# Optimization experiments

Hardware: AMD Instinct MI355X
Metric: run time of the kernel (lower is better)

Reference implementation:

```python
import jax, jax.numpy as jnp
import numpy as np

B = 128        # graphs per batch
N = 512        # nodes per graph (equal-size graphs -> dense mask all True)
F_IN = 128     # dataset.num_features
HID = 128      # hidden
C3 = 3 * HID   # num_layers * hidden (pool in_channels)
HEADS = 5
NC = 2         # num_classes
KC = NC + 1    # num_clusters2 = num_clusters_per_class*(num_classes+1) = 3
NC1 = NC       # num_clusters1 = num_clusters_per_class*num_classes = 2
OUT = 16       # pool out_channels
EPER = 8192    # edges per graph
TAU = 1.0
L1, L2 = 10.0, 0.01
BN_EPS = 1e-5


def setup_inputs() -> dict:
    key = jax.random.key(0)
    ks = jax.random.split(key, 12)
    Nn = B * N
    E = B * EPER
    x = jax.random.normal(ks[0], (Nn, F_IN), jnp.float32)
    local = jax.random.randint(ks[1], (2, E), 0, N)
    off = (jnp.repeat(jnp.arange(B), EPER) * N)[None, :]
    edge_index = (local + off).astype(jnp.int64)  # global node ids, per-graph blocks
    y = jax.random.randint(ks[2], (B,), 0, NC).astype(jnp.int64)

    def w(k_, shp, fan):
        return (jax.random.normal(k_, shp, jnp.float32) / np.sqrt(fan)).astype(jnp.float32)

    params = dict(
        W1=w(ks[3], (F_IN, HID), F_IN), b1=jnp.zeros((HID,), jnp.float32),
        W2=w(ks[4], (HID, HID), HID), b2=jnp.zeros((HID,), jnp.float32),
        W3=w(ks[5], (HID, HID), HID), b3=jnp.zeros((HID,), jnp.float32),
        bn_gamma=jnp.ones((C3,), jnp.float32), bn_beta=jnp.zeros((C3,), jnp.float32),
        k=w(ks[6], (HEADS, KC, C3), C3),
        lin_pool_W=w(ks[7], (C3, OUT), C3),
        lin1_W=w(ks[8], (NC1 * OUT, HID), NC1 * OUT), lin1_b=jnp.zeros((HID,), jnp.float32),
        lin2_W=w(ks[9], (HID, NC), HID), lin2_b=jnp.zeros((NC,), jnp.float32),
    )
    return dict(x=x, edge_index=edge_index, y=y, **params)


def reference(x, edge_index, y, W1, b1, W2, b2, W3, b3, bn_gamma, bn_beta, k,
              lin_pool_W, lin1_W, lin1_b, lin2_W, lin2_b):
    src, dst = edge_index[0], edge_index[1]
    Nn = x.shape[0]

    # GCNConv (normalize=False): out[dst] += (h @ W)[src] ; + bias
    def gcn(h, W, b):
        m = h @ W
        return jnp.zeros_like(m).at[dst].add(m[src]) + b

    h1 = jax.nn.relu(gcn(x, W1, b1))
    h2 = jax.nn.relu(gcn(h1, W2, b2))
    h3 = jax.nn.relu(gcn(h2, W3, b3))
    X = jnp.concatenate([h1, h2, h3], axis=1)  # [Nn, C3]

    # BatchNorm1d (training-mode batch stats, biased var)
    mu = X.mean(0)
    var = X.var(0)
    Xn = (X - mu) / jnp.sqrt(var + BN_EPS) * bn_gamma + bn_beta

    # --- IMPO pool ---
    H, K, C = k.shape
    k2 = k.reshape(H * K, C)
    # squared euclidean cdist: [H*K, Nn]
    d2 = jnp.maximum((k2 ** 2).sum(-1)[:, None] + (Xn ** 2).sum(-1)[None, :]
                     - 2.0 * (k2 @ Xn.T), 0.0)
    dist = (1.0 + d2 / TAU) ** (-(TAU + 1.0) / 2.0)
    dist = dist.reshape(H, K, B, N).transpose(2, 0, 3, 1)  # [B,H,N,K]
    Sh = dist / dist.sum(-1, keepdims=True)
    S = Sh.sum(1)  # sum over heads -> [B,N,K]; mask is all-True

    # per-graph adjacency aggregation: out[row] += S[col], then degree norm
    Sf = S.reshape(Nn, K)
    Sagg = jnp.zeros_like(Sf).at[src].add(Sf[dst])
    deg = (jnp.zeros((Nn,), Sf.dtype).at[src].add(1.0).at[dst].add(1.0)) / 2.0
    deg = jnp.where(deg == 0, 1.0, deg)
    S_raw = (Sagg / deg[:, None]).reshape(B, N, K)

    # use_gumbel=False path: softmax + hard argmax mask
    g = jax.nn.softmax(S_raw, axis=-1)
    onehot = jax.nn.one_hot(jnp.argmax(g, -1), K, dtype=g.dtype)
    Sfin = g * onehot

    xd = Xn.reshape(B, N, C)
    xp = jnp.einsum('bnk,bnc->bkc', Sfin, xd) @ lin_pool_W  # [B,K,OUT]
    out_x = xp[:, :NC1, :]

    # --- impo_loss ---
    yb = jnp.broadcast_to(y[:, None], (B, N))
    assigned = jnp.argmax(Sfin, -1)
    ac = assigned  # cluster_map is identity for num_clusters_per_class=1
    mr = (ac < NC) & (ac == yb)
    mw = (ac < NC) & (ac != yb)
    sum_loss = Sfin.sum(1)[:, :NC1].sum(1).mean()
    mf = (mr | mw).astype(Sfin.dtype)
    counts = jnp.zeros((NC,), Sfin.dtype).at[yb.reshape(-1)].add(mf.reshape(-1))
    bc = jnp.ones((NC,), Sfin.dtype) + counts
    weight = bc.max() / (bc + 0.001)
    logits = Sfin[..., :KC - 1]  # drop last cluster column
    logp = jax.nn.log_softmax(logits, axis=-1)
    ce = -jnp.take_along_axis(logp, yb[..., None], axis=-1)[..., 0]
    wsamp = weight[yb] * mf
    cel = (wsamp * ce).sum() / jnp.maximum(wsamp.sum(), 1e-12)
    total_loss = L1 * cel + L2 * sum_loss

    # head
    xf = out_x.reshape(B, -1)
    xf = jax.nn.relu(xf @ lin1_W + lin1_b)
    out = jax.nn.log_softmax(xf @ lin2_W + lin2_b, axis=-1)
    return (out, total_loss)
```

## Files before the change

### kernel.cpp

```cpp
#include <hip/hip_runtime.h>
#include <hip/hip_bf16.h>

#define BB 128
#define NV 512
#define NN (BB*NV)
#define EPER_C 8192
#define E_TOT (BB*EPER_C)
#define BN_EPS_F 1e-5f

typedef unsigned int u32;
typedef unsigned short u16;

__device__ __forceinline__ float bfu2f_lo(u32 w) { return __uint_as_float(w << 16); }
__device__ __forceinline__ float bfu2f_hi(u32 w) { return __uint_as_float(w & 0xFFFF0000u); }
__device__ __forceinline__ u16 f2bf(float f) {
    u32 u = __float_as_uint(f);
    u32 r = (u + 0x7FFFu + ((u >> 16) & 1u)) >> 16;
    return (u16)r;
}
__device__ __forceinline__ u32 pack2(float a, float b) {
    return (u32)f2bf(a) | ((u32)f2bf(b) << 16);
}
__device__ __forceinline__ float f16u2f(u16 h) {
    const u32 s = ((u32)h & 0x8000u) << 16;
    const u32 e = (h >> 10) & 0x1Fu;
    const u32 m = h & 0x3FFu;
    if (e == 0u) {
        float v = (float)m * 5.9604644775390625e-8f;
        return s ? -v : v;
    }
    if (e == 31u) return __uint_as_float(s | 0x7F800000u | (m << 13));
    return __uint_as_float(s | ((e + 112u) << 23) | (m << 13));
}
__device__ __forceinline__ void u32tof2(u32 w, u32 cls, float& f0, float& f1) {
    if (cls == 2u) { f0 = f16u2f((u16)(w & 0xFFFFu)); f1 = f16u2f((u16)(w >> 16)); }
    else { f0 = bfu2f_lo(w); f1 = bfu2f_hi(w); }
}
__device__ __forceinline__ float san(float v) {
    if (!(v == v)) return 0.f;
    return fminf(fmaxf(v, -1e30f), 1e30f);
}

__device__ __forceinline__ float2 h_ld2(const u32* H, size_t i2, int hf32) {
    float2 v;
    if (hf32) {
        v = ((const float2*)H)[i2];
    } else {
        const u32 w = H[i2];
        v.x = bfu2f_lo(w);
        v.y = bfu2f_hi(w);
    }
    return v;
}
__device__ __forceinline__ void h_st2(u32* H, size_t i2, float a, float b, int hf32) {
    if (hf32) {
        float2 v;
        v.x = a;
        v.y = b;
        ((float2*)H)[i2] = v;
    } else {
        H[i2] = pack2(a, b);
    }
}
__device__ __forceinline__ float h_ld1(const u32* H, size_t i, int hf32) {
    if (hf32) return ((const float*)H)[i];
    return __uint_as_float(((u32)((const u16*)H)[i]) << 16);
}

__global__ void fill_out_kernel(float* o, float v) {
    int i = blockIdx.x * 256 + threadIdx.x;
    if (i < 257) o[i] = v;
}

__global__ void init_kernel(u32* p, int n) {
    int i = blockIdx.x * 256 + threadIdx.x;
    if (i < n) p[i] = 0u;
}

__global__ void probe_kernel(const u32* g, const u32* e, u32* flags) {
    const int t = threadIdx.x;
    u32 acc = 0u;
    for (int i = t; i < 2048; i += 64) acc |= e[2 * i + 1];
#pragma unroll
    for (int s = 32; s > 0; s >>= 1) acc |= (u32)__shfl_xor((int)acc, s);
    if (t == 0) {
        const u32 w = g[0];
        u32 cls = 0u;
        if (w == 0x3F800000u) cls = 1u;
        else if (w == 0x3C003C00u) cls = 2u;
        flags[9] = cls;
        flags[8] = (acc != 0u) ? 1u : 0u;
    }
}

__device__ __forceinline__ int ld_src(const int* e, int is64, size_t i) {
    return (is64 ? e[2 * i] : e[i]) & (NN - 1);
}
__device__ __forceinline__ int ld_dst(const int* e, int is64, size_t i) {
    return (is64 ? e[2 * ((size_t)E_TOT + i)] : e[(size_t)E_TOT + i]) & (NN - 1);
}
__device__ __forceinline__ int ld_y(const int* y, int is64, int bi) {
    return (is64 ? y[2 * bi] : y[bi]) & 1;
}

#define CVT_TOT 66690
struct CvtPtrs { const void* p[14]; };
__global__ __launch_bounds__(256) void cvt_all_kernel(CvtPtrs ptrs, float* __restrict__ dst,
                                                      const u32* __restrict__ flags) {
    const int i = blockIdx.x * 256 + threadIdx.x;
    if (i >= CVT_TOT) return;
    const int kPof[14] = {0, 16384, 16512, 32896, 33024, 49408, 49536, 49920,
                          50304, 56064, 62208, 66304, 66432, 66688};
    const void* pp = ptrs.p[0];
    int base = 0;
#pragma unroll
    for (int s2 = 1; s2 < 14; ++s2) {
        if (i >= kPof[s2]) { pp = ptrs.p[s2]; base = kPof[s2]; }
    }
    const int off = i - base;
    const u32 cls = flags[9];
    float v;
    if (cls == 1u) v = ((const float*)pp)[off];
    else if (cls == 2u) v = f16u2f(((const u16*)pp)[off]);
    else v = __uint_as_float(((u32)((const u16*)pp)[off]) << 16);
    dst[i] = v;
}

__global__ __launch_bounds__(512) void csr_kernel(const int* __restrict__ eidx,
                                                  const u32* __restrict__ flags,
                                                  u16* __restrict__ sortedD,
                                                  u32* __restrict__ rpD) {
    __shared__ u32 cntD[512];
    __shared__ u32 offD[512];
    __shared__ u32 p[512];
    const int bi = blockIdx.x;
    const int t = threadIdx.x;
    const int is64 = (flags[8] == 0u);
    cntD[t] = 0u;
    __syncthreads();
    const size_t eb = (size_t)bi * EPER_C;
    for (int e = t; e < EPER_C; e += 512) {
        const int dl = ld_dst(eidx, is64, eb + e) & 511;
        atomicAdd(&cntD[dl], 1u);
    }
    __syncthreads();
    p[t] = cntD[t];
    __syncthreads();
    for (int d = 1; d < 512; d <<= 1) {
        u32 va = p[t];
        if (t >= d) va += p[t - d];
        __syncthreads();
        p[t] = va;
        __syncthreads();
    }
    offD[t] = p[t] - cntD[t];
    __syncthreads();
    rpD[bi * 513 + t] = offD[t];
    if (t == 0) rpD[bi * 513 + 512] = EPER_C;
    cntD[t] = 0u;
    __syncthreads();
    for (int e = t; e < EPER_C; e += 512) {
        const int sl = ld_src(eidx, is64, eb + e) & 511;
        const int dl = ld_dst(eidx, is64, eb + e) & 511;
        const u32 pos = offD[dl] + atomicAdd(&cntD[dl], 1u);
        sortedD[eb + pos] = (u16)sl;
    }
}

__global__ __launch_bounds__(512, 4) void gemm_k(const u32* __restrict__ X2,
                                                 const float* __restrict__ Wc,
                                                 u32* __restrict__ Y2,
                                                 const u32* __restrict__ flags,
                                                 int xmode, int hf32) {
    __shared__ float xsT[2][32][132];
    __shared__ float ws[2][32][128];
    const int n0 = blockIdx.x * 128;
    const int t = threadIdx.x;
    const int tx = t & 31, ty = t >> 5;
    u32 cls;
    if (xmode) cls = flags[9];
    else cls = hf32 ? 1u : 0u;

    float4 px[2];
    uint4 pxu;
    float4 pw[2];

#define GLOADX(kc) do { \
    if (cls == 1u) { \
        const float4* Xf4 = (const float4*)X2; \
_Pragma("unroll") \
        for (int i_ = 0; i_ < 2; ++i_) { \
            const int task = t + i_ * 512; \
            const int r_ = task >> 3, q_ = task & 7; \
            px[i_] = Xf4[(size_t)(n0 + r_) * 32 + (kc) * 8 + q_]; \
        } \
    } else { \
        const uint4* Xu4 = (const uint4*)X2; \
        const int r_ = t >> 2, uq_ = t & 3; \
        pxu = Xu4[(size_t)(n0 + r_) * 16 + (kc) * 4 + uq_]; \
    } \
} while (0)

#define GLOADW(kc) do { \
    const float4* Wf4 = (const float4*)Wc; \
_Pragma("unroll") \
    for (int i_ = 0; i_ < 2; ++i_) { \
        const int task = t + i_ * 512; \
        const int kr_ = task >> 5, cq_ = task & 31; \
        pw[i_] = Wf4[(size_t)((kc) * 32 + kr_) * 32 + cq_]; \
    } \
} while (0)

#define SWRITE(bi) do { \
    if (cls == 1u) { \
_Pragma("unroll") \
        for (int i_ = 0; i_ < 2; ++i_) { \
            const int task = t + i_ * 512; \
            const int r_ = task >> 3, q_ = task & 7; \
            xsT[bi][4 * q_ + 0][r_] = px[i_].x; \
            xsT[bi][4 * q_ + 1][r_] = px[i_].y; \
            xsT[bi][4 * q_ + 2][r_] = px[i_].z; \
            xsT[bi][4 * q_ + 3][r_] = px[i_].w; \
        } \
    } else { \
        const int r_ = t >> 2, uq_ = t & 3; \
        const u32* wp_ = (const u32*)&pxu; \
_Pragma("unroll") \
        for (int m_ = 0; m_ < 4; ++m_) { \
            float f0_, f1_; \
            u32tof2(wp_[m_], cls, f0_, f1_); \
            xsT[bi][uq_ * 8 + 2 * m_ + 0][r_] = f0_; \
            xsT[bi][uq_ * 8 + 2 * m_ + 1][r_] = f1_; \
        } \
    } \
_Pragma("unroll") \
    for (int i_ = 0; i_ < 2; ++i_) { \
        const int task = t + i_ * 512; \
        const int kr_ = task >> 5, cq_ = task & 31; \
        *(float4*)&ws[bi][kr_][4 * cq_] = pw[i_]; \
    } \
} while (0)

    GLOADX(0);
    GLOADW(0);
    SWRITE(0);
    __syncthreads();

    float a[2][4][4];
#pragma unroll
    for (int rh = 0; rh < 2; ++rh)
#pragma unroll
        for (int j = 0; j < 4; ++j)
#pragma unroll
            for (int i = 0; i < 4; ++i) a[rh][j][i] = 0.f;

    for (int c = 0; c < 4; ++c) {
        if (c < 3) {
            GLOADX(c + 1);
            GLOADW(c + 1);
        }
        const float (*xb)[132] = xsT[c & 1];
        const float (*wb)[128] = ws[c & 1];
#pragma unroll 8
        for (int k = 0; k < 32; ++k) {
            const float4 xa = *(const float4*)&xb[k][8 * ty];
            const float4 xc = *(const float4*)&xb[k][8 * ty + 4];
            const float4 wv = *(const float4*)&wb[k][4 * tx];
            const float xr0[4] = {xa.x, xa.y, xa.z, xa.w};
            const float xr1[4] = {xc.x, xc.y, xc.z, xc.w};
#pragma unroll
            for (int j = 0; j < 4; ++j) {
                a[0][j][0] += xr0[j] * wv.x;
                a[0][j][1] += xr0[j] * wv.y;
                a[0][j][2] += xr0[j] * wv.z;
                a[0][j][3] += xr0[j] * wv.w;
                a[1][j][0] += xr1[j] * wv.x;
                a[1][j][1] += xr1[j] * wv.y;
                a[1][j][2] += xr1[j] * wv.z;
                a[1][j][3] += xr1[j] * wv.w;
            }
        }
        if (c < 3) {
            SWRITE((c + 1) & 1);
            __syncthreads();
        }
    }
#undef GLOADX
#undef GLOADW
#undef SWRITE

#pragma unroll
    for (int rh = 0; rh < 2; ++rh) {
#pragma unroll
        for (int j = 0; j < 4; ++j) {
            const size_t n = (size_t)n0 + 8 * ty + 4 * rh + j;
            if (hf32) {
                float4 o;
                o.x = a[rh][j][0]; o.y = a[rh][j][1];
                o.z = a[rh][j][2]; o.w = a[rh][j][3];
                ((float4*)Y2)[n * 32 + tx] = o;
            } else {
                Y2[n * 64 + 2 * tx + 0] = pack2(a[rh][j][0], a[rh][j][1]);
                Y2[n * 64 + 2 * tx + 1] = pack2(a[rh][j][2], a[rh][j][3]);
            }
        }
    }
}

__global__ __launch_bounds__(1024) void gcn_lds_k(const u16* __restrict__ sortedD,
                                                  const u32* __restrict__ rpD,
                                                  const float* __restrict__ bias,
                                                  u32* __restrict__ M2,
                                                  float* __restrict__ bnacc,
                                                  int col_base, int hf32) {
    __shared__ float Ms[512 * 64];
    __shared__ u32 srt32[EPER_C / 2];
    __shared__ u32 rp[513];
    const int t = threadIdx.x;
    const int bi = blockIdx.x >> 1;
    const int hf = blockIdx.x & 1;
    const size_t rowbase = (size_t)bi * 512;
    const u16* srt = (const u16*)srt32;

    const u32* srcw = (const u32*)(sortedD + (size_t)bi * EPER_C);
    for (int i = t; i < EPER_C / 2; i += 1024) srt32[i] = srcw[i];
    for (int i = t; i < 513; i += 1024) rp[i] = rpD[bi * 513 + i];

    if (hf32) {
        const float4* src4 = (const float4*)M2;
        float4* dst4 = (float4*)Ms;
        for (int idx = t; idx < 512 * 16; idx += 1024) {
            const int r = idx >> 4, q = idx & 15;
            dst4[r * 16 + q] = src4[(rowbase + r) * 32 + hf * 16 + q];
        }
    } else {
        for (int idx = t; idx < 512 * 32; idx += 1024) {
            const int r = idx >> 5, q = idx & 31;
            const u32 w = M2[(rowbase + r) * 64 + hf * 32 + q];
            Ms[r * 64 + 2 * q] = bfu2f_lo(w);
            Ms[r * 64 + 2 * q + 1] = bfu2f_hi(w);
        }
    }
    __syncthreads();

    const int j = t & 15;
    const int g = t >> 4;
    const float4* M4 = (const float4*)Ms;
    const float bx = bias[hf * 64 + j * 4 + 0];
    const float by = bias[hf * 64 + j * 4 + 1];
    const float bz = bias[hf * 64 + j * 4 + 2];
    const float bw = bias[hf * 64 + j * 4 + 3];
    float S0 = 0.f, S1 = 0.f, S2 = 0.f, S3 = 0.f;
    float Q0 = 0.f, Q1 = 0.f, Q2 = 0.f, Q3 = 0.f;

#pragma unroll
    for (int gi = 0; gi < 8; ++gi) {
        const int l = g + gi * 64;
        u32 r1 = rp[l + 1];
        if (r1 > EPER_C) r1 = EPER_C;
        u32 r0 = rp[l];
        if (r0 > r1) r0 = r1;
        float ax = 0.f, ay = 0.f, az = 0.f, aw = 0.f;
        u32 idx = r0;
        for (; idx + 8 <= r1; idx += 8) {
            const int s0 = srt[idx];
            const int s1 = srt[idx + 1];
            const int s2 = srt[idx + 2];
            const int s3 = srt[idx + 3];
            const int s4 = srt[idx + 4];
            const int s5 = srt[idx + 5];
            const int s6 = srt[idx + 6];
            const int s7 = srt[idx + 7];
            const float4 v0 = M4[s0 * 16 + j];
            const float4 v1 = M4[s1 * 16 + j];
            const float4 v2 = M4[s2 * 16 + j];
            const float4 v3 = M4[s3 * 16 + j];
            const float4 v4 = M4[s4 * 16 + j];
            const float4 v5 = M4[s5 * 16 + j];
            const float4 v6 = M4[s6 * 16 + j];
            const float4 v7 = M4[s7 * 16 + j];
            ax += (v0.x + v1.x) + (v2.x + v3.x) + (v4.x + v5.x) + (v6.x + v7.x);
            ay += (v0.y + v1.y) + (v2.y + v3.y) + (v4.y + v5.y) + (v6.y + v7.y);
            az += (v0.z + v1.z) + (v2.z + v3.z) + (v4.z + v5.z) + (v6.z + v7.z);
            aw += (v0.w + v1.w) + (v2.w + v3.w) + (v4.w + v5.w) + (v6.w + v7.w);
        }
        for (; idx + 4 <= r1; idx += 4) {
            const int sa = srt[idx];
            const int sb = srt[idx + 1];
            const int sc = srt[idx + 2];
            const int sd = srt[idx + 3];
            const float4 va = M4[sa * 16 + j];
            const float4 vb = M4[sb * 16 + j];
            const float4 vc = M4[sc * 16 + j];
            const float4 vd = M4[sd * 16 + j];
            ax += va.x + vb.x; ay += va.y + vb.y; az += va.z + vb.z; aw += va.w + vb.w;
            ax += vc.x + vd.x; ay += vc.y + vd.y; az += vc.z + vd.z; aw += vc.w + vd.w;
        }
        for (; idx < r1; ++idx) {
            const int sa = srt[idx];
            const float4 va = M4[sa * 16 + j];
            ax += va.x; ay += va.y; az += va.z; aw += va.w;
        }
        float vx = san(ax + bx); vx = vx > 0.f ? vx : 0.f;
        float vy = san(ay + by); vy = vy > 0.f ? vy : 0.f;
        float vz = san(az + bz); vz = vz > 0.f ? vz : 0.f;
        float vw = san(aw + bw); vw = vw > 0.f ? vw : 0.f;
        if (hf32) {
            float4 o; o.x = vx; o.y = vy; o.z = vz; o.w = vw;
            ((float4*)M2)[(rowbase + l) * 32 + hf * 16 + j] = o;
        } else {
            const size_t pr = (rowbase + l) * 64 + hf * 32 + 2 * j;
            M2[pr] = pack2(vx, vy);
            M2[pr + 1] = pack2(vz, vw);
        }
        S0 += vx; S1 += vy; S2 += vz; S3 += vw;
        Q0 += vx * vx; Q1 += vy * vy; Q2 += vz * vz; Q3 += vw * vw;
    }

    S0 += __shfl_xor(S0, 16); Q0 += __shfl_xor(Q0, 16);
    S1 += __shfl_xor(S1, 16); Q1 += __shfl_xor(Q1, 16);
    S2 += __shfl_xor(S2, 16); Q2 += __shfl_xor(Q2, 16);
    S3 += __shfl_xor(S3, 16); Q3 += __shfl_xor(Q3, 16);
    S0 += __shfl_xor(S0, 32); Q0 += __shfl_xor(Q0, 32);
    S1 += __shfl_xor(S1, 32); Q1 += __shfl_xor(Q1, 32);
    S2 += __shfl_xor(S2, 32); Q2 += __shfl_xor(Q2, 32);
    S3 += __shfl_xor(S3, 32); Q3 += __shfl_xor(Q3, 32);

    __syncthreads();
    float* red = (float*)srt32;
    const int lane = t & 63;
    const int wid = t >> 6;
    if (lane < 16) {
        float* rw = &red[(wid * 16 + j) * 8];
        rw[0] = S0; rw[1] = Q0; rw[2] = S1; rw[3] = Q1;
        rw[4] = S2; rw[5] = Q2; rw[6] = S3; rw[7] = Q3;
    }
    __syncthreads();
    if (t < 128) {
        float s = 0.f;
        for (int w = 0; w < 16; ++w) s += red[w * 128 + t];
        const int jj = t >> 3;
        const int cc = (t >> 1) & 3;
        const int st = t & 1;
        atomicAdd(&bnacc[(size_t)(col_base + hf * 64 + jj * 4 + cc) * 2 + st], s);
    }
}

__global__ __launch_bounds__(384) void bn2_kernel(const float* __restrict__ bnacc,
                                                  const float* __restrict__ gamma,
                                                  const float* __restrict__ beta,
                                                  float* __restrict__ scaleA,
                                                  float* __restrict__ shiftA) {
    const int c = threadIdx.x;
    const float s = bnacc[c * 2 + 0];
    const float s2 = bnacc[c * 2 + 1];
    const float inv_n = 1.f / (float)NN;
    const float mu = san(s * inv_n);
    float var = san(s2 * inv_n - mu * mu);
    var = var > 0.f ? var : 0.f;
    const float sc = san(gamma[c] / sqrtf(var + BN_EPS_F));
    scaleA[c] = sc;
    shiftA[c] = san(beta[c] - mu * sc);
}

__global__ __launch_bounds__(256) void dist_kernel(const u32* __restrict__ h1,
                                                   const u32* __restrict__ h2,
                                                   const u32* __restrict__ h3,
                                                   const float* __restrict__ kc,
                                                   const float* __restrict__ scaleA,
                                                   const float* __restrict__ shiftA,
                                                   float4* __restrict__ Sf4, int hf32) {
    __shared__ float k2f[15 * 384];
    __shared__ float scl[384], shf[384];
    __shared__ float ksqp[15][16];
    __shared__ float ksq[15];
    const int t = threadIdx.x;
    for (int i = t; i < 15 * 384; i += 256) k2f[i] = kc[i];
    for (int i = t; i < 384; i += 256) {
        scl[i] = scaleA[i];
        shf[i] = shiftA[i];
    }
    __syncthreads();
    if (t < 240) {
        const int j = t >> 4, pp = t & 15;
        float q = 0.f;
        const float* kr = &k2f[j * 384 + pp * 24];
        for (int c2 = 0; c2 < 24; ++c2) {
            const float v = kr[c2];
            q += v * v;
        }
        ksqp[j][pp] = q;
    }
    __syncthreads();
    if (t < 15) {
        float q = 0.f;
#pragma unroll
        for (int pp = 0; pp < 16; ++pp) q += ksqp[t][pp];
        ksq[t] = q;
    }
    __syncthreads();
    const int n = blockIdx.x * 64 + (t >> 2);
    const int sub = t & 3;
    float acc[15];
#pragma unroll
    for (int j = 0; j < 15; ++j) acc[j] = 0.f;
    float xq = 0.f;
#pragma unroll
    for (int pL = 0; pL < 3; ++pL) {
        const u32* hp = (pL == 0) ? h1 : (pL == 1) ? h2 : h3;
        for (int q8 = sub; q8 < 16; q8 += 4) {
            float xv[8];
            if (hf32) {
                const float4 va = ((const float4*)hp)[(size_t)n * 32 + q8 * 2 + 0];
                const float4 vb = ((const float4*)hp)[(size_t)n * 32 + q8 * 2 + 1];
                xv[0] = va.x; xv[1] = va.y; xv[2] = va.z; xv[3] = va.w;
                xv[4] = vb.x; xv[5] = vb.y; xv[6] = vb.z; xv[7] = vb.w;
            } else {
                const uint4 w = ((const uint4*)hp)[(size_t)n * 16 + q8];
                xv[0] = bfu2f_lo(w.x); xv[1] = bfu2f_hi(w.x);
                xv[2] = bfu2f_lo(w.y); xv[3] = bfu2f_hi(w.y);
                xv[4] = bfu2f_lo(w.z); xv[5] = bfu2f_hi(w.z);
                xv[6] = bfu2f_lo(w.w); xv[7] = bfu2f_hi(w.w);
            }
            const int c = pL * 128 + q8 * 8;
#pragma unroll
            for (int i = 0; i < 8; ++i) {
                const float x = xv[i] * scl[c + i] + shf[c + i];
                xv[i] = x;
                xq += x * x;
            }
#pragma unroll
            for (int j = 0; j < 15; ++j) {
                const float* kr = &k2f[j * 384 + c];
                float a = acc[j];
#pragma unroll
                for (int i = 0; i < 8; ++i) a += xv[i] * kr[i];
                acc[j] = a;
            }
        }
    }
#pragma unroll
    for (int j = 0; j < 15; ++j) {
        acc[j] += __shfl_xor(acc[j], 1);
        acc[j] += __shfl_xor(acc[j], 2);
    }
    xq += __shfl_xor(xq, 1);
    xq += __shfl_xor(xq, 2);
    if (sub == 0) {
        float dist[15];
#pragma unroll
        for (int j = 0; j < 15; ++j) {
            float d2 = san(ksq[j] + xq - 2.f * acc[j]);
            d2 = d2 > 0.f ? d2 : 0.f;
            dist[j] = 1.f / (1.f + d2);
        }
        float S0 = 0.f, S1 = 0.f, S2 = 0.f;
#pragma unroll
        for (int h = 0; h < 5; ++h) {
            const float a = dist[h * 3 + 0], b = dist[h * 3 + 1], cd = dist[h * 3 + 2];
            const float inv = 1.f / fmaxf(a + b + cd, 1e-30f);
            S0 += a * inv;
            S1 += b * inv;
            S2 += cd * inv;
        }
        float4 o;
        o.x = san(S0); o.y = san(S1); o.z = san(S2); o.w = 0.f;
        Sf4[n] = o;
    }
}

__global__ __launch_bounds__(512) void sagg_kernel(const int* __restrict__ eidx,
                                                   const u32* __restrict__ flags,
                                                   const float4* __restrict__ Sf4,
                                                   const int* __restrict__ y,
                                                   int* __restrict__ nodeK,
                                                   float* __restrict__ nodeW,
                                                   float* __restrict__ scal) {
    __shared__ float sacc[512 * 3];
    __shared__ unsigned int degc[512];
    __shared__ float rA[512], rB[512];
    const int bi = blockIdx.x;
    const int t = threadIdx.x;
    const int is64 = (flags[8] == 0u);
    sacc[t] = 0.f;
    sacc[t + 512] = 0.f;
    sacc[t + 1024] = 0.f;
    degc[t] = 0u;
    __syncthreads();
    const size_t eb = (size_t)bi * EPER_C;
    for (int e = t; e < EPER_C; e += 512) {
        const int sg = ld_src(eidx, is64, eb + e);
        const int dg = ld_dst(eidx, is64, eb + e);
        const int sl = sg & 511;
        const int dl = dg & 511;
        const float4 sv = Sf4[dg];
        atomicAdd(&sacc[sl * 3 + 0], sv.x);
        atomicAdd(&sacc[sl * 3 + 1], sv.y);
        atomicAdd(&sacc[sl * 3 + 2], sv.z);
        atomicAdd(&degc[sl], 1u);
        atomicAdd(&degc[dl], 1u);
    }
    __syncthreads();
    float mfAcc = 0.f, slAcc = 0.f;
    {
        const int l = t;
        const float cnt = (float)degc[l];
        const float degf = cnt > 0.f ? cnt * 0.5f : 1.f;
        const float inv = 1.f / degf;
        const float r0 = san(sacc[l * 3 + 0] * inv);
        const float r1 = san(sacc[l * 3 + 1] * inv);
        const float r2 = san(sacc[l * 3 + 2] * inv);
        int am = 0;
        float mx = r0;
        if (r1 > mx) { mx = r1; am = 1; }
        if (r2 > mx) { mx = r2; am = 2; }
        const float e0 = expf(r0 - mx), e1 = expf(r1 - mx), e2 = expf(r2 - mx);
        const float g = san(1.f / (e0 + e1 + e2));
        const int n = bi * 512 + l;
        nodeK[n] = am;
        nodeW[n] = g;
        if (am < 2) {
            mfAcc += 1.f;
            slAcc += g;
        }
    }
    rA[t] = mfAcc;
    rB[t] = slAcc;
    __syncthreads();
    for (int sft = 256; sft > 0; sft >>= 1) {
        if (t < sft) {
            rA[t] += rA[t + sft];
            rB[t] += rB[t + sft];
        }
        __syncthreads();
    }
    if (t == 0) {
        atomicAdd(&scal[ld_y(y, is64, bi)], rA[0]);
        atomicAdd(&scal[2], rB[0]);
    }
}

__global__ __launch_bounds__(256) void ce_kernel(const int* __restrict__ nodeK,
                                                 const float* __restrict__ nodeW,
                                                 const u32* __restrict__ flags,
                                                 const int* __restrict__ y,
                                                 float* __restrict__ scal) {
    const int n = blockIdx.x * 256 + threadIdx.x;
    const int bi = n >> 9;
    const int is64 = (flags[8] == 0u);
    const int kn = nodeK[n];
    float wce = 0.f, wsum = 0.f;
    if (kn >= 0 && kn < 2) {
        const float w = nodeW[n];
        const int yb = ld_y(y, is64, bi);
        const float l0 = (kn == 0) ? w : 0.f;
        const float l1 = (kn == 1) ? w : 0.f;
        const float m = fmaxf(l0, l1);
        const float lz = m + logf(expf(l0 - m) + expf(l1 - m));
        const float ce = lz - ((yb == 0) ? l0 : l1);
        const float bc0 = 1.f + scal[0];
        const float bc1 = 1.f + scal[1];
        const float bmax = fmaxf(bc0, bc1);
        const float wt = bmax / (((yb == 0) ? bc0 : bc1) + 0.001f);
        wce = san(wt * ce);
        wsum = san(wt);
    }
    __shared__ float rA[256], rB[256];
    const int t = threadIdx.x;
    rA[t] = wce;
    rB[t] = wsum;
    __syncthreads();
    for (int sft = 128; sft > 0; sft >>= 1) {
        if (t < sft) {
            rA[t] += rA[t + sft];
            rB[t] += rB[t + sft];
        }
        __syncthreads();
    }
    if (t == 0) {
        atomicAdd(&scal[3], rA[0]);
        atomicAdd(&scal[4], rB[0]);
    }
}

__global__ __launch_bounds__(384) void xp_kernel(const u32* __restrict__ h1,
                                                 const u32* __restrict__ h2,
                                                 const u32* __restrict__ h3,
                                                 const float* __restrict__ scaleA,
                                                 const float* __restrict__ shiftA,
                                                 const int* __restrict__ nodeK,
                                                 const float* __restrict__ nodeW,
                                                 float* __restrict__ xp, int hf32) {
    __shared__ float w0s[128], w1s[128];
    __shared__ float red[4][96][8];
    const int bi = blockIdx.x >> 2;
    const int ch = blockIdx.x & 3;
    const int t = threadIdx.x;
    const int nb = bi * 512 + ch * 128;
    for (int i = t; i < 128; i += 384) {
        const int kn = nodeK[nb + i];
        const float w = nodeW[nb + i];
        w0s[i] = (kn == 0) ? w : 0.f;
        w1s[i] = (kn == 1) ? w : 0.f;
    }
    __syncthreads();
    const int a = t >> 7;
    const int l128 = t & 127;
    const int q = l128 & 31;
    const int ng = l128 >> 5;
    const u32* hp = (a == 0) ? h1 : (a == 1) ? h2 : h3;
    float ax = 0.f, ay = 0.f, az = 0.f, aw = 0.f;
    float bx = 0.f, by = 0.f, bz = 0.f, bw = 0.f;
    if (hf32) {
        const float4* h4 = (const float4*)hp;
#pragma unroll 8
        for (int l = ng; l < 128; l += 4) {
            const float4 v = h4[(size_t)(nb + l) * 32 + q];
            const float w0 = w0s[l], w1 = w1s[l];
            ax += w0 * v.x; ay += w0 * v.y; az += w0 * v.z; aw += w0 * v.w;
            bx += w1 * v.x; by += w1 * v.y; bz += w1 * v.z; bw += w1 * v.w;
        }
    } else {
        const uint2* hu = (const uint2*)hp;
#pragma unroll 8
        for (int l = ng; l < 128; l += 4) {
            const uint2 v = hu[(size_t)(nb + l) * 32 + q];
            const float w0 = w0s[l], w1 = w1s[l];
            const float x0 = bfu2f_lo(v.x), x1 = bfu2f_hi(v.x);
            const float x2 = bfu2f_lo(v.y), x3 = bfu2f_hi(v.y);
            ax += w0 * x0; ay += w0 * x1; az += w0 * x2; aw += w0 * x3;
            bx += w1 * x0; by += w1 * x1; bz += w1 * x2; bw += w1 * x3;
        }
    }
    {
        float* rw = red[ng][a * 32 + q];
        rw[0] = ax; rw[1] = ay; rw[2] = az; rw[3] = aw;
        rw[4] = bx; rw[5] = by; rw[6] = bz; rw[7] = bw;
    }
    __syncthreads();
    if (ng == 0) {
        float sw0 = 0.f, sw1 = 0.f;
        for (int i = 0; i < 128; ++i) { sw0 += w0s[i]; sw1 += w1s[i]; }
        const int col0 = a * 128 + q * 4;
        const int cq = a * 32 + q;
#pragma unroll
        for (int m = 0; m < 4; ++m) {
            const float s0 = red[0][cq][m] + red[1][cq][m] + red[2][cq][m] + red[3][cq][m];
            const float s1 = red[0][cq][4 + m] + red[1][cq][4 + m] + red[2][cq][4 + m] + red[3][cq][4 + m];
            const float sc = scaleA[col0 + m], sh = shiftA[col0 + m];
            atomicAdd(&xp[((size_t)bi * 2 + 0) * 384 + col0 + m], san(sc * s0 + sh * sw0));
            atomicAdd(&xp[((size_t)bi * 2 + 1) * 384 + col0 + m], san(sc * s1 + sh * sw1));
        }
    }
}

__global__ __launch_bounds__(128) void head_kernel(const float* __restrict__ xp,
                                                   const float* __restrict__ lpW,
                                                   const float* __restrict__ l1W,
                                                   const float* __restrict__ l1b,
                                                   const float* __restrict__ l2W,
                                                   const float* __restrict__ l2b,
                                                   float* __restrict__ outp) {
    const int bi = blockIdx.x;
    const int t = threadIdx.x;
    __shared__ float xfl[32];
    __shared__ float hidl[128];
    if (t < 32) {
        const int kk = t >> 4, o = t & 15;
        const float* xr = xp + ((size_t)bi * 2 + kk) * 384;
        float acc = 0.f;
        for (int c2 = 0; c2 < 384; ++c2) acc += xr[c2] * lpW[c2 * 16 + o];
        xfl[t] = san(acc);
    }
    __syncthreads();
    float acc = l1b[t];
    for (int i = 0; i < 32; ++i) acc += xfl[i] * l1W[i * 128 + t];
    hidl[t] = fmaxf(san(acc), 0.f);
    __syncthreads();
    if (t == 0) {
        float L0 = l2b[0], L1v = l2b[1];
        for (int j = 0; j < 128; ++j) {
            const float h = hidl[j];
            L0 += h * l2W[j * 2 + 0];
            L1v += h * l2W[j * 2 + 1];
        }
        L0 = san(L0); L1v = san(L1v);
        const float m = fmaxf(L0, L1v);
        const float ls = m + logf(expf(L0 - m) + expf(L1v - m));
        outp[bi * 2 + 0] = san(L0 - ls);
        outp[bi * 2 + 1] = san(L1v - ls);
    }
}

__global__ void fin_kernel(const float* __restrict__ scal, float* __restrict__ outp) {
    const float cel = san(scal[3] / fmaxf(scal[4], 1e-12f));
    const float total = san(10.f * cel + 0.01f * (scal[2] / (float)BB));
    outp[BB * 2] = total;
}

extern "C" void kernel_launch(void* const* d_in, const int* in_sizes, int n_in,
                              void* d_out, int out_size, void* d_ws, size_t ws_size,
                              hipStream_t stream) {
    (void)in_sizes; (void)n_in; (void)out_size;
    float* outp = (float*)d_out;

    const size_t tailW = (size_t)NN * 4 + (size_t)NN + (size_t)NN + 98304 + 16 + 768 + 768
                       + 66690 + 128 * 513 + (size_t)E_TOT / 2;
    const size_t needF = 3ull * NN * 128ull * 4ull + tailW * 4ull;
    const size_t needB = 3ull * NN * 128ull * 2ull + tailW * 4ull;
    int hf32;
    if (ws_size >= needF) hf32 = 1;
    else if (ws_size >= needB) hf32 = 0;
    else {
        fill_out_kernel<<<2, 256, 0, stream>>>(outp, 2000.f + (float)(ws_size >> 20));
        return;
    }

    const u32* xw = (const u32*)d_in[0];
    const int* eidx = (const int*)d_in[1];
    const int* y = (const int*)d_in[2];

    const size_t esz = hf32 ? 4u : 2u;
    char* base = (char*)d_ws;
    u32* H1 = (u32*)base;
    u32* H2 = (u32*)(base + (size_t)NN * 128 * esz);
    u32* H3 = (u32*)(base + 2 * (size_t)NN * 128 * esz);
    float* fb = (float*)(base + 3 * (size_t)NN * 128 * esz);
    float4* Sf4 = (float4*)fb;
    float* nodeW = fb + (size_t)NN * 4;
    int* nodeK = (int*)(nodeW + NN);
    float* xp = (float*)(nodeK + NN);
    float* scal = xp + 98304;
    u32* flags = (u32*)scal;
    float* bnacc = scal + 16;
    float* scaleA = bnacc + 768;
    float* shiftA = scaleA + 384;
    float* canon = shiftA + 384;
    u32* rpD = (u32*)(canon + 66690);
    u16* sortedD = (u16*)(rpD + 128 * 513);

    init_kernel<<<388, 256, 0, stream>>>((u32*)xp, 98304 + 16 + 768);
    probe_kernel<<<1, 64, 0, stream>>>((const u32*)d_in[9], (const u32*)eidx, flags);
    csr_kernel<<<BB, 512, 0, stream>>>(eidx, flags, sortedD, rpD);

    CvtPtrs cp;
    for (int i = 0; i < 14; ++i) cp.p[i] = d_in[3 + i];
    cvt_all_kernel<<<(CVT_TOT + 255) / 256, 256, 0, stream>>>(cp, canon, flags);

    gemm_k<<<NN / 128, 512, 0, stream>>>(xw, canon + 0, H1, flags, 1, hf32);
    gcn_lds_k<<<BB * 2, 1024, 0, stream>>>(sortedD, rpD, canon + 16384, H1, bnacc, 0, hf32);
    gemm_k<<<NN / 128, 512, 0, stream>>>(H1, canon + 16512, H2, flags, 0, hf32);
    gcn_lds_k<<<BB * 2, 1024, 0, stream>>>(sortedD, rpD, canon + 32896, H2, bnacc, 128, hf32);
    gemm_k<<<NN / 128, 512, 0, stream>>>(H2, canon + 33024, H3, flags, 0, hf32);
    gcn_lds_k<<<BB * 2, 1024, 0, stream>>>(sortedD, rpD, canon + 49408, H3, bnacc, 256, hf32);
    bn2_kernel<<<1, 384, 0, stream>>>(bnacc, canon + 49536, canon + 49920, scaleA, shiftA);
    dist_kernel<<<NN / 64, 256, 0, stream>>>(H1, H2, H3, canon + 50304, scaleA, shiftA,
                                             Sf4, hf32);
    sagg_kernel<<<BB, 512, 0, stream>>>(eidx, flags, Sf4, y, nodeK, nodeW, scal);
    ce_kernel<<<NN / 256, 256, 0, stream>>>(nodeK, nodeW, flags, y, scal);
    xp_kernel<<<BB * 4, 384, 0, stream>>>(H1, H2, H3, scaleA, shiftA, nodeK, nodeW, xp, hf32);
    head_kernel<<<BB, 128, 0, stream>>>(xp, canon + 56064, canon + 62208, canon + 66304,
                                        canon + 66432, canon + 66688, outp);
    fin_kernel<<<1, 1, 0, stream>>>(scal, outp);
}
```

Measured before the change: 419.8 us.

## Split GCN aggregation into quarter-column blocks with padded LDS and global index reads

```diff
diff --git a/kernel.cpp b/kernel.cpp
--- a/kernel.cpp
+++ b/kernel.cpp
@@ -313,45 +313,40 @@
                                                   u32* __restrict__ M2,
                                                   float* __restrict__ bnacc,
                                                   int col_base, int hf32) {
-    __shared__ float Ms[512 * 64];
-    __shared__ u32 srt32[EPER_C / 2];
+    __shared__ float Ms[512][34];
     __shared__ u32 rp[513];
+    __shared__ float red2[16][16][4];
     const int t = threadIdx.x;
-    const int bi = blockIdx.x >> 1;
-    const int hf = blockIdx.x & 1;
+    const int bi = blockIdx.x >> 2;
+    const int qd = blockIdx.x & 3;
     const size_t rowbase = (size_t)bi * 512;
-    const u16* srt = (const u16*)srt32;
-
-    const u32* srcw = (const u32*)(sortedD + (size_t)bi * EPER_C);
-    for (int i = t; i < EPER_C / 2; i += 1024) srt32[i] = srcw[i];
+
     for (int i = t; i < 513; i += 1024) rp[i] = rpD[bi * 513 + i];
 
     if (hf32) {
         const float4* src4 = (const float4*)M2;
-        float4* dst4 = (float4*)Ms;
+        for (int idx = t; idx < 512 * 8; idx += 1024) {
+            const int r = idx >> 3, q = idx & 7;
+            const float4 v = src4[(rowbase + r) * 32 + qd * 8 + q];
+            float* d = &Ms[r][4 * q];
+            d[0] = v.x; d[1] = v.y; d[2] = v.z; d[3] = v.w;
+        }
+    } else {
         for (int idx = t; idx < 512 * 16; idx += 1024) {
             const int r = idx >> 4, q = idx & 15;
-            dst4[r * 16 + q] = src4[(rowbase + r) * 32 + hf * 16 + q];
-        }
-    } else {
-        for (int idx = t; idx < 512 * 32; idx += 1024) {
-            const int r = idx >> 5, q = idx & 31;
-            const u32 w = M2[(rowbase + r) * 64 + hf * 32 + q];
-            Ms[r * 64 + 2 * q] = bfu2f_lo(w);
-            Ms[r * 64 + 2 * q + 1] = bfu2f_hi(w);
+            const u32 w = M2[(rowbase + r) * 64 + qd * 16 + q];
+            Ms[r][2 * q] = bfu2f_lo(w);
+            Ms[r][2 * q + 1] = bfu2f_hi(w);
         }
     }
     __syncthreads();
 
     const int j = t & 15;
     const int g = t >> 4;
-    const float4* M4 = (const float4*)Ms;
-    const float bx = bias[hf * 64 + j * 4 + 0];
-    const float by = bias[hf * 64 + j * 4 + 1];
-    const float bz = bias[hf * 64 + j * 4 + 2];
-    const float bw = bias[hf * 64 + j * 4 + 3];
-    float S0 = 0.f, S1 = 0.f, S2 = 0.f, S3 = 0.f;
-    float Q0 = 0.f, Q1 = 0.f, Q2 = 0.f, Q3 = 0.f;
+    const u16* srtg = sortedD + (size_t)bi * EPER_C;
+    const float b0 = bias[qd * 32 + 2 * j + 0];
+    const float b1 = bias[qd * 32 + 2 * j + 1];
+    float S0 = 0.f, S1 = 0.f, Q0 = 0.f, Q1 = 0.f;
 
 #pragma unroll
     for (int gi = 0; gi < 8; ++gi) {
@@ -360,89 +355,53 @@
         if (r1 > EPER_C) r1 = EPER_C;
         u32 r0 = rp[l];
         if (r0 > r1) r0 = r1;
-        float ax = 0.f, ay = 0.f, az = 0.f, aw = 0.f;
+        float a0 = 0.f, a1 = 0.f;
         u32 idx = r0;
         for (; idx + 8 <= r1; idx += 8) {
-            const int s0 = srt[idx];
-            const int s1 = srt[idx + 1];
-            const int s2 = srt[idx + 2];
-            const int s3 = srt[idx + 3];
-            const int s4 = srt[idx + 4];
-            const int s5 = srt[idx + 5];
-            const int s6 = srt[idx + 6];
-            const int s7 = srt[idx + 7];
-            const float4 v0 = M4[s0 * 16 + j];
-            const float4 v1 = M4[s1 * 16 + j];
-            const float4 v2 = M4[s2 * 16 + j];
-            const float4 v3 = M4[s3 * 16 + j];
-            const float4 v4 = M4[s4 * 16 + j];
-            const float4 v5 = M4[s5 * 16 + j];
-            const float4 v6 = M4[s6 * 16 + j];
-            const float4 v7 = M4[s7 * 16 + j];
-            ax += (v0.x + v1.x) + (v2.x + v3.x) + (v4.x + v5.x) + (v6.x + v7.x);
-            ay += (v0.y + v1.y) + (v2.y + v3.y) + (v4.y + v5.y) + (v6.y + v7.y);
-            az += (v0.z + v1.z) + (v2.z + v3.z) + (v4.z + v5.z) + (v6.z + v7.z);
-            aw += (v0.w + v1.w) + (v2.w + v3.w) + (v4.w + v5.w) + (v6.w + v7.w);
-        }
-        for (; idx + 4 <= r1; idx += 4) {
-            const int sa = srt[idx];
-            const int sb = srt[idx + 1];
-            const int sc = srt[idx + 2];
-            const int sd = srt[idx + 3];
-            const float4 va = M4[sa * 16 + j];
-            const float4 vb = M4[sb * 16 + j];
-            const float4 vc = M4[sc * 16 + j];
-            const float4 vd = M4[sd * 16 + j];
-            ax += va.x + vb.x; ay += va.y + vb.y; az += va.z + vb.z; aw += va.w + vb.w;
-            ax += vc.x + vd.x; ay += vc.y + vd.y; az += vc.z + vd.z; aw += vc.w + vd.w;
+            int s_[8];
+#pragma unroll
+            for (int m = 0; m < 8; ++m) s_[m] = srtg[idx + m];
+            float2 v_[8];
+#pragma unroll
+            for (int m = 0; m < 8; ++m) v_[m] = *(const float2*)&Ms[s_[m]][2 * j];
+#pragma unroll
+            for (int m = 0; m < 8; ++m) { a0 += v_[m].x; a1 += v_[m].y; }
         }
         for (; idx < r1; ++idx) {
-            const int sa = srt[idx];
-            const float4 va = M4[sa * 16 + j];
-            ax += va.x; ay += va.y; az += va.z; aw += va.w;
-        }
-        float vx = san(ax + bx); vx = vx > 0.f ? vx : 0.f;
-        float vy = san(ay + by); vy = vy > 0.f ? vy : 0.f;
-        float vz = san(az + bz); vz = vz > 0.f ? vz : 0.f;
-        float vw = san(aw + bw); vw = vw > 0.f ? vw : 0.f;
+            const int s = srtg[idx];
+            const float2 v = *(const float2*)&Ms[s][2 * j];
+            a0 += v.x; a1 += v.y;
+        }
+        float vx = san(a0 + b0); vx = vx > 0.f ? vx : 0.f;
+        float vy = san(a1 + b1); vy = vy > 0.f ? vy : 0.f;
         if (hf32) {
-            float4 o; o.x = vx; o.y = vy; o.z = vz; o.w = vw;
-            ((float4*)M2)[(rowbase + l) * 32 + hf * 16 + j] = o;
+            float2 o; o.x = vx; o.y = vy;
+            ((float2*)M2)[(rowbase + l) * 64 + qd * 16 + j] = o;
         } else {
-            const size_t pr = (rowbase + l) * 64 + hf * 32 + 2 * j;
-            M2[pr] = pack2(vx, vy);
-            M2[pr + 1] = pack2(vz, vw);
-        }
-        S0 += vx; S1 += vy; S2 += vz; S3 += vw;
-        Q0 += vx * vx; Q1 += vy * vy; Q2 += vz * vz; Q3 += vw * vw;
+            M2[(rowbase + l) * 64 + qd * 16 + j] = pack2(vx, vy);
+        }
+        S0 += vx; S1 += vy; Q0 += vx * vx; Q1 += vy * vy;
     }
 
     S0 += __shfl_xor(S0, 16); Q0 += __shfl_xor(Q0, 16);
     S1 += __shfl_xor(S1, 16); Q1 += __shfl_xor(Q1, 16);
-    S2 += __shfl_xor(S2, 16); Q2 += __shfl_xor(Q2, 16);
-    S3 += __shfl_xor(S3, 16); Q3 += __shfl_xor(Q3, 16);
     S0 += __shfl_xor(S0, 32); Q0 += __shfl_xor(Q0, 32);
     S1 += __shfl_xor(S1, 32); Q1 += __shfl_xor(Q1, 32);
-    S2 += __shfl_xor(S2, 32); Q2 += __shfl_xor(Q2, 32);
-    S3 += __shfl_xor(S3, 32); Q3 += __shfl_xor(Q3, 32);
-
-    __syncthreads();
-    float* red = (float*)srt32;
+
     const int lane = t & 63;
     const int wid = t >> 6;
     if (lane < 16) {
-        float* rw = &red[(wid * 16 + j) * 8];
-        rw[0] = S0; rw[1] = Q0; rw[2] = S1; rw[3] = Q1;
-        rw[4] = S2; rw[5] = Q2; rw[6] = S3; rw[7] = Q3;
-    }
-    __syncthreads();
-    if (t < 128) {
+        red2[wid][j][0] = S0; red2[wid][j][1] = Q0;
+        red2[wid][j][2] = S1; red2[wid][j][3] = Q1;
+    }
+    __syncthreads();
+    if (t < 64) {
+        const int jj = t >> 2;
+        const int pr = (t >> 1) & 1;
+        const int st = t & 1;
         float s = 0.f;
-        for (int w = 0; w < 16; ++w) s += red[w * 128 + t];
-        const int jj = t >> 3;
-        const int cc = (t >> 1) & 3;
-        const int st = t & 1;
-        atomicAdd(&bnacc[(size_t)(col_base + hf * 64 + jj * 4 + cc) * 2 + st], s);
+        for (int w = 0; w < 16; ++w) s += red2[w][jj][pr * 2 + st];
+        atomicAdd(&bnacc[(size_t)(col_base + qd * 32 + 2 * jj + pr) * 2 + st], s);
     }
 }
 
@@ -848,11 +807,11 @@
     cvt_all_kernel<<<(CVT_TOT + 255) / 256, 256, 0, stream>>>(cp, canon, flags);
 
     gemm_k<<<NN / 128, 512, 0, stream>>>(xw, canon + 0, H1, flags, 1, hf32);
-    gcn_lds_k<<<BB * 2, 1024, 0, stream>>>(sortedD, rpD, canon + 16384, H1, bnacc, 0, hf32);
+    gcn_lds_k<<<BB * 4, 1024, 0, stream>>>(sortedD, rpD, canon + 16384, H1, bnacc, 0, hf32);
     gemm_k<<<NN / 128, 512, 0, stream>>>(H1, canon + 16512, H2, flags, 0, hf32);
-    gcn_lds_k<<<BB * 2, 1024, 0, stream>>>(sortedD, rpD, canon + 32896, H2, bnacc, 128, hf32);
+    gcn_lds_k<<<BB * 4, 1024, 0, stream>>>(sortedD, rpD, canon + 32896, H2, bnacc, 128, hf32);
     gemm_k<<<NN / 128, 512, 0, stream>>>(H2, canon + 33024, H3, flags, 0, hf32);
-    gcn_lds_k<<<BB * 2, 1024, 0, stream>>>(sortedD, rpD, canon + 49408, H3, bnacc, 256, hf32);
+    gcn_lds_k<<<BB * 4, 1024, 0, stream>>>(sortedD, rpD, canon + 49408, H3, bnacc, 256, hf32);
     bn2_kernel<<<1, 384, 0, stream>>>(bnacc, canon + 49536, canon + 49920, scaleA, shiftA);
     dist_kernel<<<NN / 64, 256, 0, stream>>>(H1, H2, H3, canon + 50304, scaleA, shiftA,
                                              Sf4, hf32);
```

New measurement: 429.5 us. 2.3% more time.

## Build source-sorted CSR and replace atomic S aggregation with gather

Applied to the files above, without the earlier changes.

```diff
diff --git a/kernel.cpp b/kernel.cpp
--- a/kernel.cpp
+++ b/kernel.cpp
@@ -129,19 +129,26 @@
 __global__ __launch_bounds__(512) void csr_kernel(const int* __restrict__ eidx,
                                                   const u32* __restrict__ flags,
                                                   u16* __restrict__ sortedD,
-                                                  u32* __restrict__ rpD) {
+                                                  u32* __restrict__ rpD,
+                                                  u16* __restrict__ sortedS,
+                                                  u32* __restrict__ rpS) {
     __shared__ u32 cntD[512];
+    __shared__ u32 cntS[512];
     __shared__ u32 offD[512];
+    __shared__ u32 offS[512];
     __shared__ u32 p[512];
     const int bi = blockIdx.x;
     const int t = threadIdx.x;
     const int is64 = (flags[8] == 0u);
     cntD[t] = 0u;
+    cntS[t] = 0u;
     __syncthreads();
     const size_t eb = (size_t)bi * EPER_C;
     for (int e = t; e < EPER_C; e += 512) {
         const int dl = ld_dst(eidx, is64, eb + e) & 511;
+        const int sl = ld_src(eidx, is64, eb + e) & 511;
         atomicAdd(&cntD[dl], 1u);
+        atomicAdd(&cntS[sl], 1u);
     }
     __syncthreads();
     p[t] = cntD[t];
@@ -154,16 +161,33 @@
         __syncthreads();
     }
     offD[t] = p[t] - cntD[t];
+    p[t] = cntS[t];
+    __syncthreads();
+    for (int d = 1; d < 512; d <<= 1) {
+        u32 va = p[t];
+        if (t >= d) va += p[t - d];
+        __syncthreads();
+        p[t] = va;
+        __syncthreads();
+    }
+    offS[t] = p[t] - cntS[t];
     __syncthreads();
     rpD[bi * 513 + t] = offD[t];
-    if (t == 0) rpD[bi * 513 + 512] = EPER_C;
+    rpS[bi * 513 + t] = offS[t];
+    if (t == 0) {
+        rpD[bi * 513 + 512] = EPER_C;
+        rpS[bi * 513 + 512] = EPER_C;
+    }
     cntD[t] = 0u;
+    cntS[t] = 0u;
     __syncthreads();
     for (int e = t; e < EPER_C; e += 512) {
         const int sl = ld_src(eidx, is64, eb + e) & 511;
         const int dl = ld_dst(eidx, is64, eb + e) & 511;
-        const u32 pos = offD[dl] + atomicAdd(&cntD[dl], 1u);
-        sortedD[eb + pos] = (u16)sl;
+        const u32 posD = offD[dl] + atomicAdd(&cntD[dl], 1u);
+        sortedD[eb + posD] = (u16)sl;
+        const u32 posS = offS[sl] + atomicAdd(&cntS[sl], 1u);
+        sortedS[eb + posS] = (u16)dl;
     }
 }
 
@@ -569,59 +593,77 @@
     }
 }
 
-__global__ __launch_bounds__(512) void sagg_kernel(const int* __restrict__ eidx,
+__global__ __launch_bounds__(512) void sagg_kernel(const u16* __restrict__ sortedS,
+                                                   const u32* __restrict__ rpS,
+                                                   const u32* __restrict__ rpD,
                                                    const u32* __restrict__ flags,
                                                    const float4* __restrict__ Sf4,
                                                    const int* __restrict__ y,
                                                    int* __restrict__ nodeK,
                                                    float* __restrict__ nodeW,
                                                    float* __restrict__ scal) {
-    __shared__ float sacc[512 * 3];
-    __shared__ unsigned int degc[512];
+    __shared__ float sfx[512], sfy[512], sfz[512];
+    __shared__ u32 srtS32[EPER_C / 2];
+    __shared__ u32 rps[513];
+    __shared__ u32 rpd[513];
     __shared__ float rA[512], rB[512];
-    const int bi = blockIdx.x;
+    const int bi = blockIdx.x >> 1;
+    const int half = blockIdx.x & 1;
     const int t = threadIdx.x;
     const int is64 = (flags[8] == 0u);
-    sacc[t] = 0.f;
-    sacc[t + 512] = 0.f;
-    sacc[t + 1024] = 0.f;
-    degc[t] = 0u;
-    __syncthreads();
-    const size_t eb = (size_t)bi * EPER_C;
-    for (int e = t; e < EPER_C; e += 512) {
-        const int sg = ld_src(eidx, is64, eb + e);
-        const int dg = ld_dst(eidx, is64, eb + e);
-        const int sl = sg & 511;
-        const int dl = dg & 511;
-        const float4 sv = Sf4[dg];
-        atomicAdd(&sacc[sl * 3 + 0], sv.x);
-        atomicAdd(&sacc[sl * 3 + 1], sv.y);
-        atomicAdd(&sacc[sl * 3 + 2], sv.z);
-        atomicAdd(&degc[sl], 1u);
-        atomicAdd(&degc[dl], 1u);
-    }
-    __syncthreads();
+    {
+        const float4 v = Sf4[bi * 512 + t];
+        sfx[t] = v.x; sfy[t] = v.y; sfz[t] = v.z;
+    }
+    const u32* srcw = (const u32*)(sortedS + (size_t)bi * EPER_C);
+    for (int i = t; i < EPER_C / 2; i += 512) srtS32[i] = srcw[i];
+    for (int i = t; i < 513; i += 512) {
+        rps[i] = rpS[bi * 513 + i];
+        rpd[i] = rpD[bi * 513 + i];
+    }
+    __syncthreads();
+    const u16* srtS = (const u16*)srtS32;
+    const int tt = t >> 1;
+    const int sub = t & 1;
+    const int l = half * 256 + tt;
+    u32 r1 = rps[l + 1];
+    if (r1 > EPER_C) r1 = EPER_C;
+    u32 r0 = rps[l];
+    if (r0 > r1) r0 = r1;
+    const u32 degS = r1 - r0;
+    u32 d1 = rpd[l + 1];
+    if (d1 > EPER_C) d1 = EPER_C;
+    u32 d0 = rpd[l];
+    if (d0 > d1) d0 = d1;
+    const u32 degD = d1 - d0;
+    float s0 = 0.f, s1 = 0.f, s2 = 0.f;
+    for (u32 idx = r0 + sub; idx < r1; idx += 2) {
+        const int d = srtS[idx];
+        s0 += sfx[d]; s1 += sfy[d]; s2 += sfz[d];
+    }
+    s0 += __shfl_xor(s0, 1);
+    s1 += __shfl_xor(s1, 1);
+    s2 += __shfl_xor(s2, 1);
     float mfAcc = 0.f, slAcc = 0.f;
-    {
-        const int l = t;
-        const float cnt = (float)degc[l];
+    if (sub == 0) {
+        const float cnt = (float)(degS + degD);
         const float degf = cnt > 0.f ? cnt * 0.5f : 1.f;
         const float inv = 1.f / degf;
-        const float r0 = san(sacc[l * 3 + 0] * inv);
-        const float r1 = san(sacc[l * 3 + 1] * inv);
-        const float r2 = san(sacc[l * 3 + 2] * inv);
+        const float v0 = san(s0 * inv);
+        const float v1 = san(s1 * inv);
+        const float v2 = san(s2 * inv);
         int am = 0;
-        float mx = r0;
-        if (r1 > mx) { mx = r1; am = 1; }
-        if (r2 > mx) { mx = r2; am = 2; }
-        const float e0 = expf(r0 - mx), e1 = expf(r1 - mx), e2 = expf(r2 - mx);
+        float mx = v0;
+        if (v1 > mx) { mx = v1; am = 1; }
+        if (v2 > mx) { mx = v2; am = 2; }
+        const float e0 = expf(v0 - mx), e1 = expf(v1 - mx), e2 = expf(v2 - mx);
         const float g = san(1.f / (e0 + e1 + e2));
         const int n = bi * 512 + l;
         nodeK[n] = am;
         nodeW[n] = g;
         if (am < 2) {
-            mfAcc += 1.f;
-            slAcc += g;
+            mfAcc = 1.f;
+            slAcc = g;
         }
     }
     rA[t] = mfAcc;
@@ -805,7 +847,7 @@
     float* outp = (float*)d_out;
 
     const size_t tailW = (size_t)NN * 4 + (size_t)NN + (size_t)NN + 98304 + 16 + 768 + 768
-                       + 66690 + 128 * 513 + (size_t)E_TOT / 2;
+                       + 66690 + 2 * (128 * 513) + 2 * ((size_t)E_TOT / 2);
     const size_t needF = 3ull * NN * 128ull * 4ull + tailW * 4ull;
     const size_t needB = 3ull * NN * 128ull * 2ull + tailW * 4ull;
     int hf32;
@@ -838,10 +880,12 @@
     float* canon = shiftA + 384;
     u32* rpD = (u32*)(canon + 66690);
     u16* sortedD = (u16*)(rpD + 128 * 513);
+    u32* rpS = (u32*)(sortedD + E_TOT);
+    u16* sortedS = (u16*)(rpS + 128 * 513);
 
     init_kernel<<<388, 256, 0, stream>>>((u32*)xp, 98304 + 16 + 768);
     probe_kernel<<<1, 64, 0, stream>>>((const u32*)d_in[9], (const u32*)eidx, flags);
-    csr_kernel<<<BB, 512, 0, stream>>>(eidx, flags, sortedD, rpD);
+    csr_kernel<<<BB, 512, 0, stream>>>(eidx, flags, sortedD, rpD, sortedS, rpS);
 
     CvtPtrs cp;
     for (int i = 0; i < 14; ++i) cp.p[i] = d_in[3 + i];
@@ -856,7 +900,8 @@
     bn2_kernel<<<1, 384, 0, stream>>>(bnacc, canon + 49536, canon + 49920, scaleA, shiftA);
     dist_kernel<<<NN / 64, 256, 0, stream>>>(H1, H2, H3, canon + 50304, scaleA, shiftA,
                                              Sf4, hf32);
-    sagg_kernel<<<BB, 512, 0, stream>>>(eidx, flags, Sf4, y, nodeK, nodeW, scal);
+    sagg_kernel<<<BB * 2, 512, 0, stream>>>(sortedS, rpS, rpD, flags, Sf4, y,
+                                            nodeK, nodeW, scal);
     ce_kernel<<<NN / 256, 256, 0, stream>>>(nodeK, nodeW, flags, y, scal);
     xp_kernel<<<BB * 4, 384, 0, stream>>>(H1, H2, H3, scaleA, shiftA, nodeK, nodeW, xp, hf32);
     head_kernel<<<BB, 128, 0, stream>>>(xp, canon + 56064, canon + 62208, canon + 66304,
```

Result: faster. 406.4 us (-3.2%).
